# Optimization experiments

Measured on AMD Instinct MI355X. Metric: run time of the kernel, lower is better.

Reference implementation:

```python
import jax, jax.numpy as jnp
from jax import lax
import numpy as np

TOPK = 100
SCALE = 4.0
EXCEPT_THRESH = 0.01

B, C, H, W = 16, 80, 256, 256


def setup_inputs() -> dict:
    key = jax.random.key(0)
    k1, k2, k3 = jax.random.split(key, 3)
    heatmap = jax.random.uniform(k1, (B, C, H, W), dtype=jnp.float32)
    offset = jax.random.normal(k2, (B, 2, H, W), dtype=jnp.float32)
    wh = jax.random.uniform(k3, (B, 2, H, W), dtype=jnp.float32)
    return {"heatmap": heatmap, "offset": offset, "wh": wh}


def reference(heatmap, offset, wh):
    b, c, h, w = heatmap.shape
    # 3x3 max-pool NMS: keep only local peaks
    pooled = lax.reduce_window(heatmap, -jnp.inf, lax.max,
                               (1, 1, 3, 3), (1, 1, 1, 1), "SAME")
    keep = (pooled == heatmap).astype(heatmap.dtype)
    hm = keep * heatmap
    # top-k over all classes x spatial positions
    flat = hm.reshape(b, -1)                      # [B, C*H*W]
    scores, indices = lax.top_k(flat, TOPK)       # [B, K]
    scores = scores[:, :, None]                   # [B, K, 1]
    ids = (indices // (h * w)).astype(jnp.float32)[:, :, None]
    spatial = indices % (h * w)                   # [B, K] flat spatial index
    topk_ys = (spatial // w).astype(jnp.float32)
    topk_xs = (spatial % w).astype(jnp.float32)
    # gather offset / wh at peak locations
    off = offset.transpose(0, 2, 3, 1).reshape(b, -1, 2)   # [B, H*W, 2]
    whr = wh.transpose(0, 2, 3, 1).reshape(b, -1, 2)       # [B, H*W, 2]
    off_g = jnp.take_along_axis(off, spatial[:, :, None], axis=1)  # [B, K, 2]
    wh_g = jnp.take_along_axis(whr, spatial[:, :, None], axis=1)   # [B, K, 2]
    cx = topk_xs + off_g[:, :, 0]
    cy = topk_ys + off_g[:, :, 1]
    half_w = wh_g[:, :, 0] * 0.5
    half_h = wh_g[:, :, 1] * 0.5
    bboxes = jnp.stack([cx - half_w, cy - half_h, cx + half_w, cy + half_h], axis=-1)  # [B, K, 4]
    # mask out low-score detections with -1
    mask = scores > EXCEPT_THRESH                 # [B, K, 1]
    neg1 = jnp.float32(-1.0)
    ids = jnp.where(mask, ids, neg1)
    scores = jnp.where(mask, scores, neg1)
    bboxes = jnp.where(mask, bboxes, neg1)
    return ids, scores, bboxes * SCALE
```

## Files before the change

kernel.cpp:

```cpp
#include <hip/hip_runtime.h>
#include <stdint.h>

#define HB 16
#define HC 80
#define HH 256
#define HWD 256
#define PLANE (HH * HWD)
#define NPLANES (HB * HC)
#define K_TOP 100
#define CAP 2048
#define OUTCAP 256
#define NEG_INF (-3.402823466e38f)

__device__ __forceinline__ int blockReduceSum(int v, int* sred) {
    for (int off = 32; off > 0; off >>= 1) v += __shfl_down(v, off);
    int t = threadIdx.x;
    __syncthreads();
    if ((t & 63) == 0) sred[t >> 6] = v;
    __syncthreads();
    return sred[0] + sred[1] + sred[2] + sred[3];
}

__device__ __forceinline__ bool better(float a, int ai, float b, int bi) {
    return (a > b) || (a == b && ai < bi);
}

__device__ void bitonic256(float* sv, int* si) {
    int t = threadIdx.x;
    for (unsigned k = 2; k <= 256; k <<= 1) {
        for (unsigned j = k >> 1; j > 0; j >>= 1) {
            __syncthreads();
            unsigned i = (unsigned)t, x = i ^ j;
            if (x > i) {
                float a = sv[i], bv = sv[x];
                int ai = si[i], bi = si[x];
                bool sw = ((i & k) == 0) ? better(bv, bi, a, ai) : better(a, ai, bv, bi);
                if (sw) { sv[i] = bv; si[i] = bi; sv[x] = a; si[x] = ai; }
            }
        }
    }
    __syncthreads();
}

__device__ __forceinline__ float4 loadrow(const float* __restrict__ pl, int r, int lane) {
    int rc = min(max(r, 0), HH - 1);
    float4 v = ((const float4*)(pl + rc * HWD))[lane];
    if (r != rc) { v.x = NEG_INF; v.y = NEG_INF; v.z = NEG_INF; v.w = NEG_INF; }
    return v;
}

__device__ __forceinline__ float4 hmax4(float4 v, int lane) {
    float vl = __shfl_up(v.w, 1);
    float vr = __shfl_down(v.x, 1);
    if (lane == 0) vl = NEG_INF;
    if (lane == 63) vr = NEG_INF;
    float4 h;
    h.x = fmaxf(fmaxf(vl, v.x), v.y);
    h.y = fmaxf(fmaxf(v.x, v.y), v.z);
    h.z = fmaxf(fmaxf(v.y, v.z), v.w);
    h.w = fmaxf(fmaxf(v.z, v.w), vr);
    return h;
}

__global__ __launch_bounds__(256) void k_plane_topk(const float* __restrict__ heat,
                                                    float* __restrict__ wsv,
                                                    int* __restrict__ wsi) {
    int plane = blockIdx.x;
    int c = plane % HC;
    const float* pl = heat + (size_t)plane * PLANE;
    int t = threadIdx.x;
    int lane = t & 63;
    int rs = (t >> 6) << 6;

    __shared__ float bufv[CAP];
    __shared__ int   bufi[CAP];
    __shared__ float outv[OUTCAP];
    __shared__ int   outi[OUTCAP];
    __shared__ int   cnt, cnt2;
    __shared__ int   sred[4];

    float thr = 0.98f;
    int n = 0;
    for (int attempt = 0; attempt < 3; ++attempt) {
        if (t == 0) cnt = 0;
        __syncthreads();

        float4 rm1 = loadrow(pl, rs - 1, lane);
        float4 r0  = loadrow(pl, rs, lane);
        float4 hA = hmax4(rm1, lane);
        float4 hB = hmax4(r0, lane);
        float4 vB = r0;

        for (int i = 0; i < 64; i += 4) {
            float4 n0 = loadrow(pl, rs + i + 1, lane);
            float4 n1 = loadrow(pl, rs + i + 2, lane);
            float4 n2 = loadrow(pl, rs + i + 3, lane);
            float4 n3 = loadrow(pl, rs + i + 4, lane);
#pragma unroll
            for (int u = 0; u < 4; ++u) {
                float4 nr = (u == 0) ? n0 : (u == 1) ? n1 : (u == 2) ? n2 : n3;
                int row = rs + i + u;
                float4 hC = hmax4(nr, lane);
                float p0 = fmaxf(fmaxf(hA.x, hB.x), hC.x);
                float p1 = fmaxf(fmaxf(hA.y, hB.y), hC.y);
                float p2 = fmaxf(fmaxf(hA.z, hB.z), hC.z);
                float p3 = fmaxf(fmaxf(hA.w, hB.w), hC.w);
                int colb = lane << 2;
                if (vB.x >= p0 && vB.x > thr) {
                    int p = atomicAdd(&cnt, 1);
                    if (p < CAP) { bufv[p] = vB.x; bufi[p] = (c << 16) | (row << 8) | colb; }
                }
                if (vB.y >= p1 && vB.y > thr) {
                    int p = atomicAdd(&cnt, 1);
                    if (p < CAP) { bufv[p] = vB.y; bufi[p] = (c << 16) | (row << 8) | (colb + 1); }
                }
                if (vB.z >= p2 && vB.z > thr) {
                    int p = atomicAdd(&cnt, 1);
                    if (p < CAP) { bufv[p] = vB.z; bufi[p] = (c << 16) | (row << 8) | (colb + 2); }
                }
                if (vB.w >= p3 && vB.w > thr) {
                    int p = atomicAdd(&cnt, 1);
                    if (p < CAP) { bufv[p] = vB.w; bufi[p] = (c << 16) | (row << 8) | (colb + 3); }
                }
                hA = hB; hB = hC; vB = nr;
            }
        }
        __syncthreads();
        n = cnt;
        __syncthreads();
        if (n >= K_TOP && n <= CAP) break;
        if (n > CAP) thr = 1.0f - (1.0f - thr) * 0.25f;
        else thr = (attempt == 0) ? 0.5f : 0.01f;
    }
    int nn = min(n, CAP);

    float regv[CAP / 256];
#pragma unroll
    for (int k = 0; k < CAP / 256; ++k) {
        int s = t + (k << 8);
        regv[k] = (s < nn) ? bufv[s] : NEG_INF;
    }

    float T100;
    if (nn >= K_TOP) {
        unsigned lo = 0u, hi = 0x7f800000u;
        while (hi - lo > 1u) {
            unsigned mid = (lo + hi) >> 1u;
            float mv = __uint_as_float(mid);
            int cl = 0;
#pragma unroll
            for (int k = 0; k < CAP / 256; ++k) cl += (regv[k] >= mv) ? 1 : 0;
            int tot = blockReduceSum(cl, sred);
            if (tot >= K_TOP) lo = mid; else hi = mid;
        }
        T100 = __uint_as_float(lo);
    } else {
        T100 = NEG_INF;
    }

    outv[t] = NEG_INF; outi[t] = 0x7fffffff;
    if (t == 0) cnt2 = 0;
    __syncthreads();
#pragma unroll
    for (int k = 0; k < CAP / 256; ++k) {
        int s = t + (k << 8);
        if (s < nn && bufv[s] >= T100) {
            int p = atomicAdd(&cnt2, 1);
            if (p < OUTCAP) { outv[p] = bufv[s]; outi[p] = bufi[s]; }
        }
    }
    __syncthreads();
    int c2 = cnt2;
    if (c2 > K_TOP) bitonic256(outv, outi);
    __syncthreads();
    if (t < K_TOP) {
        wsv[plane * K_TOP + t] = outv[t];
        wsi[plane * K_TOP + t] = outi[t];
    }
}

__global__ __launch_bounds__(256) void k_batch_out(const float* __restrict__ wsv,
                                                   const int* __restrict__ wsi,
                                                   const float* __restrict__ offset,
                                                   const float* __restrict__ wh,
                                                   float* __restrict__ out) {
    int b = blockIdx.x;
    int t = threadIdx.x;
    const int NCAND = HC * K_TOP;
    const float* v_in = wsv + b * NCAND;
    const int*   i_in = wsi + b * NCAND;

    __shared__ float outv[OUTCAP];
    __shared__ int   outi[OUTCAP];
    __shared__ int   cnt2;
    __shared__ int   sred[4];

    float regv[32];
#pragma unroll
    for (int k = 0; k < 32; ++k) {
        int s = t + (k << 8);
        regv[k] = (s < NCAND) ? v_in[s] : NEG_INF;
    }
    int cl0 = 0;
#pragma unroll
    for (int k = 0; k < 32; ++k) cl0 += (regv[k] > NEG_INF) ? 1 : 0;
    int nreal = blockReduceSum(cl0, sred);

    float T100;
    if (nreal >= K_TOP) {
        unsigned lo = 0u, hi = 0x7f800000u;
        while (hi - lo > 1u) {
            unsigned mid = (lo + hi) >> 1u;
            float mv = __uint_as_float(mid);
            int cl = 0;
#pragma unroll
            for (int k = 0; k < 32; ++k) cl += (regv[k] >= mv) ? 1 : 0;
            int tot = blockReduceSum(cl, sred);
            if (tot >= K_TOP) lo = mid; else hi = mid;
        }
        T100 = __uint_as_float(lo);
    } else {
        T100 = NEG_INF;
    }

    outv[t] = NEG_INF; outi[t] = 0x7fffffff;
    if (t == 0) cnt2 = 0;
    __syncthreads();
#pragma unroll
    for (int k = 0; k < 32; ++k) {
        int s = t + (k << 8);
        if (s < NCAND && regv[k] >= T100 && regv[k] > NEG_INF) {
            int p = atomicAdd(&cnt2, 1);
            if (p < OUTCAP) { outv[p] = regv[k]; outi[p] = i_in[s]; }
        }
    }
    __syncthreads();
    bitonic256(outv, outi);

    if (t < K_TOP) {
        float val = outv[t];
        int idx = outi[t];
        bool valid = val > 0.01f;
        int cch = idx >> 16;
        int spatial = idx & 0xFFFF;
        int y = spatial >> 8, x = spatial & 0xFF;
        const float* offb = offset + (size_t)b * 2 * PLANE;
        const float* whb  = wh     + (size_t)b * 2 * PLANE;
        float o0 = offb[spatial], o1 = offb[PLANE + spatial];
        float w0 = whb[spatial],  w1 = whb[PLANE + spatial];
        float cx = (float)x + o0, cy = (float)y + o1;
        float hw = w0 * 0.5f, hh = w1 * 0.5f;
        int g = b * K_TOP + t;
        out[g]                = valid ? (float)cch : -1.0f;
        out[HB * K_TOP + g]   = valid ? val        : -1.0f;
        float b0 = valid ? (cx - hw) : -1.0f;
        float b1 = valid ? (cy - hh) : -1.0f;
        float b2 = valid ? (cx + hw) : -1.0f;
        float b3 = valid ? (cy + hh) : -1.0f;
        float* bb = out + 2 * HB * K_TOP + 4 * g;
        bb[0] = b0 * 4.0f; bb[1] = b1 * 4.0f; bb[2] = b2 * 4.0f; bb[3] = b3 * 4.0f;
    }
}

extern "C" void kernel_launch(void* const* d_in, const int* in_sizes, int n_in,
                              void* d_out, int out_size, void* d_ws, size_t ws_size,
                              hipStream_t stream) {
    (void)in_sizes; (void)n_in; (void)out_size; (void)ws_size;
    const float* heat   = (const float*)d_in[0];
    const float* offset = (const float*)d_in[1];
    const float* wh     = (const float*)d_in[2];
    float* out = (float*)d_out;
    float* wsv = (float*)d_ws;
    int*   wsi = (int*)((char*)d_ws + (size_t)NPLANES * K_TOP * sizeof(float));

    k_plane_topk<<<NPLANES, 256, 0, stream>>>(heat, wsv, wsi);
    k_batch_out<<<HB, 256, 0, stream>>>(wsv, wsi, offset, wh, out);
}
```

Measured before the change: 509.3 us.

## Prefetch next row group, drop boundary clamps, and narrow threshold binary search ranges

Restructures the per-plane NMS scan so the next four rows are loaded while the current four are processed (software prefetch), and uses unclamped row loads except at the bottom edge. The per-pixel atomics now sit behind one combined predicate. The binary searches for the 100th-largest score start from the candidate threshold (or the max of per-plane 100th scores) with an upper bound of just above 1.0, which cuts search iterations. This bound relies on heatmap values lying in [0,1]. The bitonic sort now always runs instead of only when more than 100 candidates exist.

New measurement: 511.7 us. No clear change (+0.5%).

```diff
diff --git a/kernel.cpp b/kernel.cpp
--- a/kernel.cpp
+++ b/kernel.cpp
@@ -42,10 +42,14 @@
     __syncthreads();
 }
 
-__device__ __forceinline__ float4 loadrow(const float* __restrict__ pl, int r, int lane) {
-    int rc = min(max(r, 0), HH - 1);
+__device__ __forceinline__ float4 loadrow_u(const float* __restrict__ pl, int r, int lane) {
+    return ((const float4*)(pl + r * HWD))[lane];
+}
+
+__device__ __forceinline__ float4 loadrow_g(const float* __restrict__ pl, int r, int lane) {
+    int rc = min(r, HH - 1);
     float4 v = ((const float4*)(pl + rc * HWD))[lane];
-    if (r != rc) { v.x = NEG_INF; v.y = NEG_INF; v.z = NEG_INF; v.w = NEG_INF; }
+    if (r >= HH) { v.x = NEG_INF; v.y = NEG_INF; v.z = NEG_INF; v.w = NEG_INF; }
     return v;
 }
 
@@ -70,7 +74,7 @@
     const float* pl = heat + (size_t)plane * PLANE;
     int t = threadIdx.x;
     int lane = t & 63;
-    int rs = (t >> 6) << 6;
+    int rs = __builtin_amdgcn_readfirstlane((t >> 6) << 6);
 
     __shared__ float bufv[CAP];
     __shared__ int   bufi[CAP];
@@ -85,42 +89,49 @@
         if (t == 0) cnt = 0;
         __syncthreads();
 
-        float4 rm1 = loadrow(pl, rs - 1, lane);
-        float4 r0  = loadrow(pl, rs, lane);
+        float4 rm1 = loadrow_u(pl, max(rs - 1, 0), lane);
+        float4 r0  = loadrow_u(pl, rs, lane);
+        float4 n0 = loadrow_u(pl, rs + 1, lane);
+        float4 n1 = loadrow_u(pl, rs + 2, lane);
+        float4 n2 = loadrow_u(pl, rs + 3, lane);
+        float4 n3 = loadrow_u(pl, rs + 4, lane);
+        if (rs == 0) { rm1.x = NEG_INF; rm1.y = NEG_INF; rm1.z = NEG_INF; rm1.w = NEG_INF; }
         float4 hA = hmax4(rm1, lane);
         float4 hB = hmax4(r0, lane);
         float4 vB = r0;
 
-        for (int i = 0; i < 64; i += 4) {
-            float4 n0 = loadrow(pl, rs + i + 1, lane);
-            float4 n1 = loadrow(pl, rs + i + 2, lane);
-            float4 n2 = loadrow(pl, rs + i + 3, lane);
-            float4 n3 = loadrow(pl, rs + i + 4, lane);
+        for (int j = 0; j < 16; ++j) {
+            float4 c0 = n0, c1 = n1, c2 = n2, c3 = n3;
+            if (j < 15) {
+                int rb = rs + 4 * j + 5;
+                n0 = loadrow_u(pl, rb, lane);
+                n1 = loadrow_u(pl, rb + 1, lane);
+                n2 = loadrow_u(pl, rb + 2, lane);
+                n3 = loadrow_g(pl, rb + 3, lane);
+            }
 #pragma unroll
             for (int u = 0; u < 4; ++u) {
-                float4 nr = (u == 0) ? n0 : (u == 1) ? n1 : (u == 2) ? n2 : n3;
-                int row = rs + i + u;
+                float4 nr = (u == 0) ? c0 : (u == 1) ? c1 : (u == 2) ? c2 : c3;
+                int row = rs + 4 * j + u;
                 float4 hC = hmax4(nr, lane);
                 float p0 = fmaxf(fmaxf(hA.x, hB.x), hC.x);
                 float p1 = fmaxf(fmaxf(hA.y, hB.y), hC.y);
                 float p2 = fmaxf(fmaxf(hA.z, hB.z), hC.z);
                 float p3 = fmaxf(fmaxf(hA.w, hB.w), hC.w);
-                int colb = lane << 2;
-                if (vB.x >= p0 && vB.x > thr) {
-                    int p = atomicAdd(&cnt, 1);
-                    if (p < CAP) { bufv[p] = vB.x; bufi[p] = (c << 16) | (row << 8) | colb; }
-                }
-                if (vB.y >= p1 && vB.y > thr) {
-                    int p = atomicAdd(&cnt, 1);
-                    if (p < CAP) { bufv[p] = vB.y; bufi[p] = (c << 16) | (row << 8) | (colb + 1); }
-                }
-                if (vB.z >= p2 && vB.z > thr) {
-                    int p = atomicAdd(&cnt, 1);
-                    if (p < CAP) { bufv[p] = vB.z; bufi[p] = (c << 16) | (row << 8) | (colb + 2); }
-                }
-                if (vB.w >= p3 && vB.w > thr) {
-                    int p = atomicAdd(&cnt, 1);
-                    if (p < CAP) { bufv[p] = vB.w; bufi[p] = (c << 16) | (row << 8) | (colb + 3); }
+                bool k0 = (vB.x >= p0) && (vB.x > thr);
+                bool k1 = (vB.y >= p1) && (vB.y > thr);
+                bool k2 = (vB.z >= p2) && (vB.z > thr);
+                bool k3 = (vB.w >= p3) && (vB.w > thr);
+                if (k0 | k1 | k2 | k3) {
+                    int colb = lane << 2;
+                    if (k0) { int p = atomicAdd(&cnt, 1);
+                        if (p < CAP) { bufv[p] = vB.x; bufi[p] = (c << 16) | (row << 8) | colb; } }
+                    if (k1) { int p = atomicAdd(&cnt, 1);
+                        if (p < CAP) { bufv[p] = vB.y; bufi[p] = (c << 16) | (row << 8) | (colb + 1); } }
+                    if (k2) { int p = atomicAdd(&cnt, 1);
+                        if (p < CAP) { bufv[p] = vB.z; bufi[p] = (c << 16) | (row << 8) | (colb + 2); } }
+                    if (k3) { int p = atomicAdd(&cnt, 1);
+                        if (p < CAP) { bufv[p] = vB.w; bufi[p] = (c << 16) | (row << 8) | (colb + 3); } }
                 }
                 hA = hB; hB = hC; vB = nr;
             }
@@ -143,7 +154,7 @@
 
     float T100;
     if (nn >= K_TOP) {
-        unsigned lo = 0u, hi = 0x7f800000u;
+        unsigned lo = __float_as_uint(thr), hi = 0x3F800001u;
         while (hi - lo > 1u) {
             unsigned mid = (lo + hi) >> 1u;
             float mv = __uint_as_float(mid);
@@ -170,9 +181,7 @@
         }
     }
     __syncthreads();
-    int c2 = cnt2;
-    if (c2 > K_TOP) bitonic256(outv, outi);
-    __syncthreads();
+    bitonic256(outv, outi);
     if (t < K_TOP) {
         wsv[plane * K_TOP + t] = outv[t];
         wsi[plane * K_TOP + t] = outi[t];
@@ -194,6 +203,7 @@
     __shared__ int   outi[OUTCAP];
     __shared__ int   cnt2;
     __shared__ int   sred[4];
+    __shared__ float smaxw[4];
 
     float regv[32];
 #pragma unroll
@@ -206,9 +216,17 @@
     for (int k = 0; k < 32; ++k) cl0 += (regv[k] > NEG_INF) ? 1 : 0;
     int nreal = blockReduceSum(cl0, sred);
 
+    float m = NEG_INF;
+    if (t < HC) m = v_in[t * K_TOP + K_TOP - 1];
+    for (int off = 32; off > 0; off >>= 1) m = fmaxf(m, __shfl_down(m, off));
+    if ((t & 63) == 0) smaxw[t >> 6] = m;
+    __syncthreads();
+    float smax = fmaxf(fmaxf(smaxw[0], smaxw[1]), fmaxf(smaxw[2], smaxw[3]));
+
     float T100;
     if (nreal >= K_TOP) {
-        unsigned lo = 0u, hi = 0x7f800000u;
+        unsigned lo = (smax > 0.0f) ? __float_as_uint(smax) : 0u;
+        unsigned hi = 0x3F800001u;
         while (hi - lo > 1u) {
             unsigned mid = (lo + hi) >> 1u;
             float mv = __uint_as_float(mid);
```
